# Kernel optimization log

Measured on AMD Instinct MI355X. Metric: run time of the kernel, lower is better.

## Reference

```python
import jax, jax.numpy as jnp
import numpy as np

B, S, D = 4, 1024, 1024
E, F, TOPK = 16, 512, 4


def setup_inputs() -> dict:
    key = jax.random.key(0)
    k1, k2, k3, k4, k5 = jax.random.split(key, 5)
    scale = 0.02
    return {
        "x": jax.random.normal(k1, (B, S, D), dtype=jnp.float32),
        "Wr": jax.random.normal(k2, (D, E), dtype=jnp.float32) * scale,   # router
        "Wg": jax.random.normal(k3, (E, D, F), dtype=jnp.float32) * scale,  # gate proj
        "Wu": jax.random.normal(k4, (E, D, F), dtype=jnp.float32) * scale,  # up proj
        "Wd": jax.random.normal(k5, (E, F, D), dtype=jnp.float32) * scale,  # down proj
    }


def reference(x, Wr, Wg, Wu, Wd):
    b, s, d = x.shape
    xf = x.reshape(-1, d)                      # [N, D], N = B*S
    n = xf.shape[0]
    e = Wr.shape[1]

    # --- router: softmax over experts, top-k, renormalized weights ---
    probs = jax.nn.softmax(xf @ Wr, axis=-1)   # [N, E]
    w, idx = jax.lax.top_k(probs, TOPK)        # [N, K], [N, K]
    w = w / jnp.sum(w, axis=-1, keepdims=True)

    # combine weights per (token, expert); zero for unselected experts.
    # Equivalent to the per-expert where/gather/scatter-add loop in torch.
    cw = jnp.zeros((n, e), dtype=xf.dtype).at[jnp.arange(n)[:, None], idx].add(w)

    # --- per-expert gated FFN (SwiGLU), combined with routing weights ---
    def body(acc, ws):
        wg, wu, wd, c = ws                     # [D,F], [D,F], [F,D], [N]
        h = jax.nn.silu(xf @ wg) * (xf @ wu)   # [N, F]
        return acc + c[:, None] * (h @ wd), None

    out, _ = jax.lax.scan(body, jnp.zeros_like(xf), (Wg, Wu, Wd, cw.T))
    return out.reshape(b, s, d)
```

## Files before the change

kernel.cpp:

```cpp
#include <hip/hip_runtime.h>

#define N_TOK 4096
#define DIM   1024
#define NE    16
#define NF    512
#define TOPK  4
#define CAP   4096
#define NPAIR (N_TOK * TOPK)
#define MAXTILES 144
#define GU_BLOCKS (8 * MAXTILES)
#define DN_BLOCKS (8 * MAXTILES)
#define PREPD_BLOCKS (NE * 128)
#define RP_ROUTER 1024
#define RP_PREP   4096

typedef _Float16 v8h __attribute__((ext_vector_type(8)));
typedef float    v4f __attribute__((ext_vector_type(4)));

__device__ __forceinline__ void prep_tile(
    const float* __restrict__ src, unsigned short* __restrict__ dst,
    int R, int C, int RIL, int e, int cbl, int rbl, float (*tile)[65])
{
    int c0 = cbl * 64, r0 = rbl * 64;
    const float* s = src + (size_t)e * R * C;
    int t = threadIdx.x;
    int tr = t >> 4, tc = (t & 15) * 4;
#pragma unroll
    for (int i = 0; i < 4; i++) {
        int row = i * 16 + tr;
        float4 v = *(const float4*)(s + (size_t)(r0 + row) * C + c0 + tc);
        tile[row][tc + 0] = v.x; tile[row][tc + 1] = v.y;
        tile[row][tc + 2] = v.z; tile[row][tc + 3] = v.w;
    }
    __syncthreads();
    int ktPerE = R >> 5;
    int cbPerE = C >> RIL;
    int imgSz  = (1 << RIL) * 32;
#pragma unroll
    for (int i = 0; i < 4; i++) {
        int nr = i * 16 + tr;
        int orow = c0 + nr;
        int k0 = r0 + tc;
        int cb = orow >> RIL;
        int r  = orow & ((1 << RIL) - 1);
        int kt = k0 >> 5;
        size_t off = ((size_t)(e * cbPerE + cb) * ktPerE + kt) * imgSz
                   + r * 32 + (k0 & 31);
        union { unsigned short u[4]; uint2 v; } p;
#pragma unroll
        for (int j = 0; j < 4; j++)
            p.u[j] = __builtin_bit_cast(unsigned short, (_Float16)tile[tc + j][nr]);
        *(uint2*)(dst + off) = p.v;
    }
}

__global__ __launch_bounds__(256) void router_prep_kernel(
    const float* __restrict__ x, const float* __restrict__ Wr,
    const float* __restrict__ Wg, const float* __restrict__ Wu,
    int* __restrict__ tokIdx, float* __restrict__ tokW,
    unsigned short* __restrict__ xb,
    unsigned short* __restrict__ Wg_t, unsigned short* __restrict__ Wu_t)
{
    __shared__ __align__(16) float tile[64][65];
    int bid = blockIdx.x;
    if (bid >= RP_ROUTER) {
        int pid = bid - RP_ROUTER;
        int z = pid >> 7;
        int which = z >> 4, e = z & 15;
        int bx = pid & 127;
        int cbl = bx & 7, rbl = bx >> 3;
        prep_tile(which ? Wu : Wg, which ? Wu_t : Wg_t,
                  DIM, NF, 6, e, cbl, rbl, tile);
        return;
    }
    int tid = threadIdx.x;
    int w = tid >> 6, l = tid & 63;
    int t = bid * 4 + w;

    double z[NE];
#pragma unroll
    for (int e = 0; e < NE; e++) z[e] = 0.0;
    const float* xrow = x + (size_t)t * DIM;
#pragma unroll
    for (int i = 0; i < 16; i++) {
        int d = i * 64 + l;
        double xv = (double)xrow[d];
        const float4* wr = (const float4*)(Wr + d * NE);
        float4 w0 = wr[0], w1 = wr[1], w2 = wr[2], w3 = wr[3];
        z[0]  += xv * w0.x; z[1]  += xv * w0.y; z[2]  += xv * w0.z; z[3]  += xv * w0.w;
        z[4]  += xv * w1.x; z[5]  += xv * w1.y; z[6]  += xv * w1.z; z[7]  += xv * w1.w;
        z[8]  += xv * w2.x; z[9]  += xv * w2.y; z[10] += xv * w2.z; z[11] += xv * w2.w;
        z[12] += xv * w3.x; z[13] += xv * w3.y; z[14] += xv * w3.z; z[15] += xv * w3.w;
    }
    const float4* xv4 = (const float4*)xrow;
#pragma unroll
    for (int h2 = 0; h2 < 2; h2++) {
        int base = h2 * 512 + l * 8;
        float4 a = xv4[h2 * 128 + l * 2];
        float4 b = xv4[h2 * 128 + l * 2 + 1];
        union { unsigned short u[8]; uint4 v; } p;
        p.u[0] = __builtin_bit_cast(unsigned short, (_Float16)a.x);
        p.u[1] = __builtin_bit_cast(unsigned short, (_Float16)a.y);
        p.u[2] = __builtin_bit_cast(unsigned short, (_Float16)a.z);
        p.u[3] = __builtin_bit_cast(unsigned short, (_Float16)a.w);
        p.u[4] = __builtin_bit_cast(unsigned short, (_Float16)b.x);
        p.u[5] = __builtin_bit_cast(unsigned short, (_Float16)b.y);
        p.u[6] = __builtin_bit_cast(unsigned short, (_Float16)b.z);
        p.u[7] = __builtin_bit_cast(unsigned short, (_Float16)b.w);
        *(uint4*)(xb + (size_t)t * DIM + base) = p.v;
    }
#pragma unroll
    for (int e = 0; e < NE; e++) {
#pragma unroll
        for (int m = 1; m < 64; m <<= 1) z[e] += __shfl_xor(z[e], m, 64);
    }
    if (l == 0) {
        bool taken[NE];
#pragma unroll
        for (int e = 0; e < NE; e++) taken[e] = false;
        int idx[TOPK]; double sel[TOPK];
        for (int k = 0; k < TOPK; k++) {
            int bi = 0; double bv = -1.0e300;
            for (int e = 0; e < NE; e++)
                if (!taken[e] && z[e] > bv) { bv = z[e]; bi = e; }
            taken[bi] = true; idx[k] = bi; sel[k] = bv;
        }
        double m = sel[0];
        double ex[TOPK]; double s = 0.0;
        for (int k = 0; k < TOPK; k++) { ex[k] = exp(sel[k] - m); s += ex[k]; }
        for (int k = 0; k < TOPK; k++) {
            tokIdx[t * TOPK + k] = idx[k];
            tokW[t * TOPK + k]   = (float)(ex[k] / s);
        }
    }
}

__global__ __launch_bounds__(256) void bin_kernel(
    const int* __restrict__ tokIdx,
    int* __restrict__ cnt, int* __restrict__ bpair)
{
    int e = blockIdx.x;
    int tid = threadIdx.x, lane = tid & 63, wv = tid >> 6;
    __shared__ int wsum[4];
    __shared__ int sbase;
    if (tid == 0) sbase = 0;
    __syncthreads();
    unsigned long long lt = (1ULL << lane) - 1ULL;
#pragma unroll 1
    for (int c0 = 0; c0 < NPAIR; c0 += 1024) {
        int i0 = c0 + tid * 4;
        int4 v = *(const int4*)(tokIdx + i0);
        int m[4] = {v.x == e, v.y == e, v.z == e, v.w == e};
        int r[4]; int wcnt = 0;
#pragma unroll
        for (int j = 0; j < 4; j++) {
            unsigned long long bal = __ballot(m[j] != 0);
            r[j] = wcnt + __popcll(bal & lt);
            wcnt += __popcll(bal);
        }
        if (lane == 0) wsum[wv] = wcnt;
        __syncthreads();
        int woff = sbase;
        for (int k = 0; k < wv; k++) woff += wsum[k];
#pragma unroll
        for (int j = 0; j < 4; j++)
            if (m[j]) bpair[e * CAP + woff + r[j]] = i0 + j;
        __syncthreads();
        if (tid == 0) sbase += wsum[0] + wsum[1] + wsum[2] + wsum[3];
        __syncthreads();
    }
    if (tid == 0) cnt[e] = sbase;
}

__device__ __forceinline__ int ldsw(int row, int chunk) {
    return row * 32 + (chunk ^ ((row >> 1) & 3)) * 8;
}

__device__ __forceinline__ void gload16(const unsigned short* g, unsigned short* l) {
    __builtin_amdgcn_global_load_lds(
        (const __attribute__((address_space(1))) void*)g,
        (__attribute__((address_space(3))) void*)l, 16, 0, 0);
}

__device__ __forceinline__ bool find_tile(const int* __restrict__ cnt,
                                          int ti, int& e, int& mt, int& tbase) {
    int rt = 0;
#pragma unroll 1
    for (int ee = 0; ee < NE; ee++) {
        int nt = (cnt[ee] + 127) >> 7;
        if (ti < rt + nt) { e = ee; mt = ti - rt; tbase = rt; return true; }
        rt += nt;
    }
    return false;
}

__global__ __launch_bounds__(256) void ffn_gate_up_kernel(
    const unsigned short* __restrict__ xb,
    const unsigned short* __restrict__ Wg_t,
    const unsigned short* __restrict__ Wu_t,
    const int* __restrict__ cnt,
    const int* __restrict__ bpair,
    unsigned short* __restrict__ h_t,
    const float* __restrict__ Wd,
    unsigned short* __restrict__ Wd_t)
{
    __shared__ __align__(16) unsigned char smem[32768];
    unsigned short* sX = (unsigned short*)smem;
    unsigned short* sG = (unsigned short*)(smem + 16384);
    unsigned short* sU = (unsigned short*)(smem + 24576);
    float (*tile)[65] = (float (*)[65])smem;

    int bid = blockIdx.x;
    if (bid >= GU_BLOCKS) {
        int pid = bid - GU_BLOCKS;
        int e = pid >> 7;
        int bx = pid & 127;
        int cbl = bx & 15, rbl = bx >> 4;
        prep_tile(Wd, Wd_t, NF, DIM, 7, e, cbl, rbl, tile);
        return;
    }
    int xcd = bid & 7, q = bid >> 3;
    int ti = xcd * 18 + (q >> 3);
    int fb = q & 7;
    int e, mt, tbase;
    if (!find_tile(cnt, ti, e, mt, tbase)) return;
    int count = cnt[e];

    int tid = threadIdx.x, lane = tid & 63, w = tid >> 6;

    int srow0 = w * 16 + (lane >> 2);
    int srow1 = srow0 + 64;
    int spos  = lane & 3;
    int cx0 = spos ^ ((srow0 >> 1) & 3);
    int cx1 = spos ^ ((srow1 >> 1) & 3);
    int tok0 = bpair[e * CAP + min(mt * 128 + srow0, count - 1)] >> 2;
    int tok1 = bpair[e * CAP + min(mt * 128 + srow1, count - 1)] >> 2;
    const unsigned short* gX0 = xb + (size_t)tok0 * DIM + cx0 * 8;
    const unsigned short* gX1 = xb + (size_t)tok1 * DIM + cx1 * 8;
    const unsigned short* gG  = Wg_t + ((size_t)(e * 8 + fb) * 32) * 2048 + srow0 * 32 + cx0 * 8;
    const unsigned short* gU  = Wu_t + ((size_t)(e * 8 + fb) * 32) * 2048 + srow0 * 32 + cx0 * 8;
    unsigned short* dX0 = sX + (size_t)(w * 16) * 32;
    unsigned short* dX1 = sX + (size_t)(64 + w * 16) * 32;
    unsigned short* dG  = sG + (size_t)(w * 16) * 32;
    unsigned short* dU  = sU + (size_t)(w * 16) * 32;

    int row = lane & 15, q2 = lane >> 4;
    int rw = w & 1, cw = w >> 1;
    int aoff[4], goff[2];
#pragma unroll
    for (int mi = 0; mi < 4; mi++) aoff[mi] = ldsw(rw * 64 + mi * 16 + row, q2);
#pragma unroll
    for (int ni = 0; ni < 2; ni++) goff[ni] = ldsw(cw * 32 + ni * 16 + row, q2);

    v4f accG[4][2], accU[4][2];
    v4f zero = {0.f, 0.f, 0.f, 0.f};
#pragma unroll
    for (int mi = 0; mi < 4; mi++)
#pragma unroll
        for (int ni = 0; ni < 2; ni++) { accG[mi][ni] = zero; accU[mi][ni] = zero; }

#define STAGE_GU(b, kt) do {                                   \
        gload16(gX0 + (kt) * 32, dX0 + (b) * 4096);            \
        gload16(gX1 + (kt) * 32, dX1 + (b) * 4096);            \
        gload16(gG + (size_t)(kt) * 2048, dG + (b) * 2048);    \
        gload16(gU + (size_t)(kt) * 2048, dU + (b) * 2048);    \
    } while (0)

    STAGE_GU(0, 0);
    __syncthreads();

#pragma unroll 1
    for (int kt = 0; kt < 32; kt++) {
        int buf = kt & 1;
        if (kt < 31) STAGE_GU(buf ^ 1, kt + 1);
        const unsigned short* bX = sX + buf * 4096;
        const unsigned short* bGp = sG + buf * 2048;
        const unsigned short* bUp = sU + buf * 2048;
        v8h a[4], bg[2], bu[2];
#pragma unroll
        for (int mi = 0; mi < 4; mi++) a[mi] = *(const v8h*)&bX[aoff[mi]];
#pragma unroll
        for (int ni = 0; ni < 2; ni++) {
            bg[ni] = *(const v8h*)&bGp[goff[ni]];
            bu[ni] = *(const v8h*)&bUp[goff[ni]];
        }
#pragma unroll
        for (int mi = 0; mi < 4; mi++)
#pragma unroll
            for (int ni = 0; ni < 2; ni++) {
                accG[mi][ni] = __builtin_amdgcn_mfma_f32_16x16x32_f16(a[mi], bg[ni], accG[mi][ni], 0, 0, 0);
                accU[mi][ni] = __builtin_amdgcn_mfma_f32_16x16x32_f16(a[mi], bu[ni], accU[mi][ni], 0, 0, 0);
            }
        __syncthreads();
    }
#undef STAGE_GU

    size_t himg = (size_t)(tbase + mt) * 16;
#pragma unroll
    for (int mi = 0; mi < 4; mi++)
#pragma unroll
        for (int ni = 0; ni < 2; ni++) {
            int f = fb * 64 + cw * 32 + ni * 16 + row;
#pragma unroll
            for (int i = 0; i < 4; i++) {
                int rl = rw * 64 + mi * 16 + q2 * 4 + i;
                int pos = mt * 128 + rl;
                if (pos < count) {
                    float gv = accG[mi][ni][i];
                    float uv = accU[mi][ni][i];
                    float hv = gv * uv / (1.0f + __expf(-gv));
                    size_t off = (himg + (f >> 5)) * 4096 + rl * 32 + (f & 31);
                    h_t[off] = __builtin_bit_cast(unsigned short, (_Float16)hv);
                }
            }
        }
}

__global__ __launch_bounds__(256) void ffn_down_kernel(
    const unsigned short* __restrict__ h_t,
    const unsigned short* __restrict__ Wd_t,
    const int* __restrict__ cnt,
    const int* __restrict__ bpair,
    unsigned short* __restrict__ part)
{
    int bid = blockIdx.x;
    int xcd = bid & 7, q = bid >> 3;
    int ti = xcd * 18 + (q >> 3);
    int db = q & 7;
    int e, mt, tbase;
    if (!find_tile(cnt, ti, e, mt, tbase)) return;
    int count = cnt[e];

    __shared__ __align__(16) unsigned short sH[2 * 128 * 32];
    __shared__ __align__(16) unsigned short sW[2 * 128 * 32];

    int tid = threadIdx.x, lane = tid & 63, w = tid >> 6;

    int srow0 = w * 16 + (lane >> 2);
    int srow1 = srow0 + 64;
    int spos  = lane & 3;
    int c0 = spos ^ ((srow0 >> 1) & 3);
    int c1 = spos ^ ((srow1 >> 1) & 3);
    const unsigned short* hbase = h_t + ((size_t)(tbase + mt) * 16) * 4096;
    const unsigned short* wbase = Wd_t + ((size_t)(e * 8 + db) * 16) * 4096;
    const unsigned short* gH0 = hbase + srow0 * 32 + c0 * 8;
    const unsigned short* gH1 = hbase + srow1 * 32 + c1 * 8;
    const unsigned short* gW0 = wbase + srow0 * 32 + c0 * 8;
    const unsigned short* gW1 = wbase + srow1 * 32 + c1 * 8;
    unsigned short* dH0 = sH + (size_t)(w * 16) * 32;
    unsigned short* dH1 = sH + (size_t)(64 + w * 16) * 32;
    unsigned short* dW0 = sW + (size_t)(w * 16) * 32;
    unsigned short* dW1 = sW + (size_t)(64 + w * 16) * 32;

    int row = lane & 15, q2 = lane >> 4;
    int rw = w & 1, cw = w >> 1;
    int aoff[4], boff[4];
#pragma unroll
    for (int mi = 0; mi < 4; mi++) aoff[mi] = ldsw(rw * 64 + mi * 16 + row, q2);
#pragma unroll
    for (int ni = 0; ni < 4; ni++) boff[ni] = ldsw(cw * 64 + ni * 16 + row, q2);

    v4f acc[4][4];
    v4f zero = {0.f, 0.f, 0.f, 0.f};
#pragma unroll
    for (int mi = 0; mi < 4; mi++)
#pragma unroll
        for (int ni = 0; ni < 4; ni++) acc[mi][ni] = zero;

#define STAGE_D(b, kt) do {                                         \
        gload16(gH0 + (size_t)(kt) * 4096, dH0 + (b) * 4096);       \
        gload16(gH1 + (size_t)(kt) * 4096, dH1 + (b) * 4096);       \
        gload16(gW0 + (size_t)(kt) * 4096, dW0 + (b) * 4096);       \
        gload16(gW1 + (size_t)(kt) * 4096, dW1 + (b) * 4096);       \
    } while (0)

    STAGE_D(0, 0);
    __syncthreads();

#pragma unroll 1
    for (int kt = 0; kt < 16; kt++) {
        int buf = kt & 1;
        if (kt < 15) STAGE_D(buf ^ 1, kt + 1);
        const unsigned short* bH = sH + buf * 4096;
        const unsigned short* bW = sW + buf * 4096;
        v8h a[4], b[4];
#pragma unroll
        for (int mi = 0; mi < 4; mi++) a[mi] = *(const v8h*)&bH[aoff[mi]];
#pragma unroll
        for (int ni = 0; ni < 4; ni++) b[ni] = *(const v8h*)&bW[boff[ni]];
#pragma unroll
        for (int mi = 0; mi < 4; mi++)
#pragma unroll
            for (int ni = 0; ni < 4; ni++)
                acc[mi][ni] = __builtin_amdgcn_mfma_f32_16x16x32_f16(a[mi], b[ni], acc[mi][ni], 0, 0, 0);
        __syncthreads();
    }
#undef STAGE_D

#pragma unroll
    for (int mi = 0; mi < 4; mi++)
#pragma unroll
        for (int i = 0; i < 4; i++) {
            int rl = rw * 64 + mi * 16 + q2 * 4 + i;
            int pos = mt * 128 + rl;
            if (pos < count) {
                int p = bpair[e * CAP + pos];
#pragma unroll
                for (int ni = 0; ni < 4; ni++) {
                    int col = db * 128 + cw * 64 + ni * 16 + row;
                    part[(size_t)p * DIM + col] =
                        __builtin_bit_cast(unsigned short, (_Float16)acc[mi][ni][i]);
                }
            }
        }
}

__global__ __launch_bounds__(256) void combine_kernel(
    const unsigned short* __restrict__ part, const float* __restrict__ tokW,
    float* __restrict__ out)
{
    int gid = blockIdx.x * 256 + threadIdx.x;
    int t = gid >> 8;
    int c = (gid & 255) * 4;
    float4 r = {0.f, 0.f, 0.f, 0.f};
#pragma unroll
    for (int k = 0; k < TOPK; k++) {
        float wk = tokW[t * TOPK + k];
        union { uint2 u; _Float16 h[4]; } cv;
        cv.u = *(const uint2*)(part + ((size_t)(t * TOPK + k)) * DIM + c);
        r.x += wk * (float)cv.h[0];
        r.y += wk * (float)cv.h[1];
        r.z += wk * (float)cv.h[2];
        r.w += wk * (float)cv.h[3];
    }
    *(float4*)(out + (size_t)t * DIM + c) = r;
}

extern "C" void kernel_launch(void* const* d_in, const int* in_sizes, int n_in,
                              void* d_out, int out_size, void* d_ws, size_t ws_size,
                              hipStream_t stream)
{
    const float* x  = (const float*)d_in[0];
    const float* Wr = (const float*)d_in[1];
    const float* Wg = (const float*)d_in[2];
    const float* Wu = (const float*)d_in[3];
    const float* Wd = (const float*)d_in[4];
    float* out = (float*)d_out;
    char* ws = (char*)d_ws;

    size_t off = 0;
    int* tokIdx = (int*)(ws + off);   off += (size_t)NPAIR * 4;
    float* tokW = (float*)(ws + off); off += (size_t)NPAIR * 4;
    int* cnt    = (int*)(ws + off);   off += 256;
    int* bpair  = (int*)(ws + off);   off += (size_t)NE * CAP * 4;
    unsigned short* xb   = (unsigned short*)(ws + off); off += (size_t)N_TOK * DIM * 2;
    unsigned short* Wg_t = (unsigned short*)(ws + off); off += (size_t)NE * DIM * NF * 2;
    unsigned short* Wu_t = (unsigned short*)(ws + off); off += (size_t)NE * DIM * NF * 2;
    unsigned short* Wd_t = (unsigned short*)(ws + off); off += (size_t)NE * DIM * NF * 2;
    unsigned short* h_t  = (unsigned short*)(ws + off); off += (size_t)MAXTILES * 16 * 4096 * 2;
    unsigned short* part = (unsigned short*)(ws + off); off += (size_t)NPAIR * DIM * 2;

    router_prep_kernel<<<RP_ROUTER + RP_PREP, 256, 0, stream>>>(
        x, Wr, Wg, Wu, tokIdx, tokW, xb, Wg_t, Wu_t);
    bin_kernel<<<NE, 256, 0, stream>>>(tokIdx, cnt, bpair);
    ffn_gate_up_kernel<<<GU_BLOCKS + PREPD_BLOCKS, 256, 0, stream>>>(
        xb, Wg_t, Wu_t, cnt, bpair, h_t, Wd, Wd_t);
    ffn_down_kernel<<<DN_BLOCKS, 256, 0, stream>>>(
        h_t, Wd_t, cnt, bpair, part);
    combine_kernel<<<(N_TOK * DIM) / (256 * 4), 256, 0, stream>>>(part, tokW, out);
}
```

Baseline: 269.4 us.

## Triple-buffer LDS staging with explicit vmcnt waits in gate-up and down GEMMs

Both expert GEMM kernels move from double to triple buffering of shared-memory tiles, keeping two K-tiles of global-to-LDS loads in flight. Each iteration now waits on a partial vmcnt count followed by raw s_barrier and sched_barrier calls instead of __syncthreads. The aim is to hide global load latency behind MFMA work. In exchange, LDS per block grows to 48KB, which may reduce occupancy, and correctness now rests on the hand-counted vmcnt values matching the number of loads per stage.

```diff
diff --git a/kernel.cpp b/kernel.cpp
--- a/kernel.cpp
+++ b/kernel.cpp
@@ -204,10 +204,10 @@
     const float* __restrict__ Wd,
     unsigned short* __restrict__ Wd_t)
 {
-    __shared__ __align__(16) unsigned char smem[32768];
+    __shared__ __align__(16) unsigned char smem[49152];
     unsigned short* sX = (unsigned short*)smem;
-    unsigned short* sG = (unsigned short*)(smem + 16384);
-    unsigned short* sU = (unsigned short*)(smem + 24576);
+    unsigned short* sG = (unsigned short*)(smem + 24576);
+    unsigned short* sU = (unsigned short*)(smem + 36864);
     float (*tile)[65] = (float (*)[65])smem;
 
     int bid = blockIdx.x;
@@ -267,12 +267,21 @@
     } while (0)
 
     STAGE_GU(0, 0);
-    __syncthreads();
+    STAGE_GU(1, 1);
 
 #pragma unroll 1
     for (int kt = 0; kt < 32; kt++) {
-        int buf = kt & 1;
-        if (kt < 31) STAGE_GU(buf ^ 1, kt + 1);
+        int buf = kt % 3;
+        if (kt < 30) {
+            STAGE_GU((kt + 2) % 3, kt + 2);
+            asm volatile("s_waitcnt vmcnt(8)" ::: "memory");
+        } else if (kt == 30) {
+            asm volatile("s_waitcnt vmcnt(4)" ::: "memory");
+        } else {
+            asm volatile("s_waitcnt vmcnt(0)" ::: "memory");
+        }
+        __builtin_amdgcn_s_barrier();
+        __builtin_amdgcn_sched_barrier(0);
         const unsigned short* bX = sX + buf * 4096;
         const unsigned short* bGp = sG + buf * 2048;
         const unsigned short* bUp = sU + buf * 2048;
@@ -291,7 +300,9 @@
                 accG[mi][ni] = __builtin_amdgcn_mfma_f32_16x16x32_f16(a[mi], bg[ni], accG[mi][ni], 0, 0, 0);
                 accU[mi][ni] = __builtin_amdgcn_mfma_f32_16x16x32_f16(a[mi], bu[ni], accU[mi][ni], 0, 0, 0);
             }
-        __syncthreads();
+        __builtin_amdgcn_sched_barrier(0);
+        __builtin_amdgcn_s_barrier();
+        __builtin_amdgcn_sched_barrier(0);
     }
 #undef STAGE_GU
 
@@ -331,8 +342,8 @@
     if (!find_tile(cnt, ti, e, mt, tbase)) return;
     int count = cnt[e];
 
-    __shared__ __align__(16) unsigned short sH[2 * 128 * 32];
-    __shared__ __align__(16) unsigned short sW[2 * 128 * 32];
+    __shared__ __align__(16) unsigned short sH[3 * 128 * 32];
+    __shared__ __align__(16) unsigned short sW[3 * 128 * 32];
 
     int tid = threadIdx.x, lane = tid & 63, w = tid >> 6;
 
@@ -375,12 +386,21 @@
     } while (0)
 
     STAGE_D(0, 0);
-    __syncthreads();
+    STAGE_D(1, 1);
 
 #pragma unroll 1
     for (int kt = 0; kt < 16; kt++) {
-        int buf = kt & 1;
-        if (kt < 15) STAGE_D(buf ^ 1, kt + 1);
+        int buf = kt % 3;
+        if (kt < 14) {
+            STAGE_D((kt + 2) % 3, kt + 2);
+            asm volatile("s_waitcnt vmcnt(8)" ::: "memory");
+        } else if (kt == 14) {
+            asm volatile("s_waitcnt vmcnt(4)" ::: "memory");
+        } else {
+            asm volatile("s_waitcnt vmcnt(0)" ::: "memory");
+        }
+        __builtin_amdgcn_s_barrier();
+        __builtin_amdgcn_sched_barrier(0);
         const unsigned short* bH = sH + buf * 4096;
         const unsigned short* bW = sW + buf * 4096;
         v8h a[4], b[4];
@@ -393,7 +413,9 @@
 #pragma unroll
             for (int ni = 0; ni < 4; ni++)
                 acc[mi][ni] = __builtin_amdgcn_mfma_f32_16x16x32_f16(a[mi], b[ni], acc[mi][ni], 0, 0, 0);
-        __syncthreads();
+        __builtin_amdgcn_sched_barrier(0);
+        __builtin_amdgcn_s_barrier();
+        __builtin_amdgcn_sched_barrier(0);
     }
 #undef STAGE_D
 
```

Measured after the change: 269.9 us. No clear change (+0.2%).
